# Kernel optimization log

Hardware: AMD Instinct MI355X
Metric: run time of the kernel (lower is better)

The kernel has to match this reference:

```python
import jax, jax.numpy as jnp
import numpy as np

N_NODES = 50000
N_EDGES = 500000
D = 128
R = 8
L = 2
BN_EPS = 1e-5


def setup_inputs() -> dict:
    key = jax.random.key(0)
    ks = jax.random.split(key, 8)
    x = jax.random.normal(ks[0], (N_NODES, D), dtype=jnp.float32)
    xe = jax.random.normal(ks[1], (N_EDGES, D), dtype=jnp.float32)
    edge_index = jax.random.randint(ks[2], (2, N_EDGES), 0, N_NODES, dtype=jnp.int64)
    edge_type = jax.random.randint(ks[3], (N_EDGES,), 0, R, dtype=jnp.int64)
    # glorot init for weight/root, zeros bias; BN affine params
    w_scale = jnp.sqrt(6.0 / (D + D))
    weight = jax.random.uniform(ks[4], (L, R, D, D), jnp.float32, -w_scale, w_scale)
    root = jax.random.uniform(ks[5], (L, D, D), jnp.float32, -w_scale, w_scale)
    bias = jnp.zeros((L, D), jnp.float32)
    bn_gamma = jnp.ones((L, D), jnp.float32)
    bn_beta = jnp.zeros((L, D), jnp.float32)
    return {"x": x, "xe": xe, "edge_index": edge_index, "edge_type": edge_type,
            "weight": weight, "root": root, "bias": bias,
            "bn_gamma": bn_gamma, "bn_beta": bn_beta}


def _rgcn_edge_conv(h, xe, src, dst, etype, w, rt, b):
    # message: relu(x_j + xe) per edge (independent of relation mask)
    m = jax.nn.relu(h[src] + xe)                         # [E, D]
    # mean-aggregate per (relation, dst) via a combined segment id
    n = h.shape[0]
    seg = etype * n + dst                                # [E]
    sums = jax.ops.segment_sum(m, seg, num_segments=R * n)            # [R*N, D]
    cnt = jax.ops.segment_sum(jnp.ones((m.shape[0],), m.dtype), seg,
                              num_segments=R * n)                     # [R*N]
    mean = sums / jnp.maximum(cnt, 1.0)[:, None]
    hr = mean.reshape(R, n, -1)                          # [R, N, D]
    out = jnp.einsum('rnd,rdo->no', hr, w)               # sum_i H_i @ W_i
    out = out + h @ rt + b
    return out


def _batch_norm(h, gamma, beta):
    mu = h.mean(axis=0)
    var = jnp.mean((h - mu) ** 2, axis=0)  # biased, as torch BN (training)
    return (h - mu) * jax.lax.rsqrt(var + BN_EPS) * gamma + beta


def reference(x, xe, edge_index, edge_type, weight, root, bias, bn_gamma, bn_beta):
    src, dst = edge_index[0], edge_index[1]
    h = x
    for l in range(L):
        h = _rgcn_edge_conv(h, xe, src, dst, edge_type, weight[l], root[l], bias[l])
        h = _batch_norm(h, bn_gamma[l], bn_beta[l])
        if l != L - 1:
            h = jax.nn.relu(h)
        # drop_ratio=0 -> dropout is identity
    return h  # JK='last'
```

## Files before the change

### kernel.cpp

```cpp
#include <hip/hip_runtime.h>
#include <hip/hip_bf16.h>

typedef __attribute__((ext_vector_type(8))) short bf16x8;
typedef __attribute__((ext_vector_type(4))) float f32x4;

constexpr int D = 128;
constexpr int R = 8;
constexpr float BN_EPS = 1e-5f;

__device__ __forceinline__ unsigned short f2bf(float x) {
  __hip_bfloat16 b = __float2bfloat16(x);
  union { __hip_bfloat16 b; unsigned short u; } c; c.b = b; return c.u;
}

__global__ __launch_bounds__(256) void hist_k(const int* __restrict__ ei,
                                              const int* __restrict__ et,
                                              int* __restrict__ cnt, int E) {
  int e = blockIdx.x * 256 + threadIdx.x;
  if (e >= E) return;
  atomicAdd(&cnt[ei[E + e] * 8 + et[e]], 1);
}

__global__ __launch_bounds__(256) void scan_partial_k(const int* __restrict__ cnt,
                                                      int* __restrict__ offs,
                                                      int* __restrict__ bsum, int NK) {
  __shared__ int s[256];
  int tid = threadIdx.x;
  int base = blockIdx.x * 4096 + tid * 16;
  int loc[16];
  int sum = 0;
  #pragma unroll
  for (int i = 0; i < 16; ++i) {
    int idx = base + i;
    int v = (idx < NK) ? cnt[idx] : 0;
    loc[i] = sum; sum += v;
  }
  s[tid] = sum;
  __syncthreads();
  if (tid == 0) {
    int run = 0;
    for (int i = 0; i < 256; ++i) { int t = s[i]; s[i] = run; run += t; }
    bsum[blockIdx.x] = run;
  }
  __syncthreads();
  int off = s[tid];
  #pragma unroll
  for (int i = 0; i < 16; ++i) {
    int idx = base + i;
    if (idx < NK) offs[idx] = off + loc[i];
  }
}

__global__ void scan_bsums_k(int* __restrict__ bsum, int nb) {
  if (threadIdx.x == 0 && blockIdx.x == 0) {
    int run = 0;
    for (int b = 0; b < nb; ++b) { int t = bsum[b]; bsum[b] = run; run += t; }
  }
}

__global__ __launch_bounds__(256) void scan_addback_k(int* __restrict__ offs,
                                                      const int* __restrict__ bsum,
                                                      int NK, int E) {
  int idx = blockIdx.x * 256 + threadIdx.x;
  if (idx < NK) offs[idx] += bsum[idx >> 12];
  if (idx == 0) offs[NK] = E;
}

__global__ __launch_bounds__(256) void place_k(const int* __restrict__ ei,
                                               const int* __restrict__ et,
                                               const int* __restrict__ offs,
                                               int* __restrict__ cnt,
                                               int2* __restrict__ pairs, int E) {
  int e = blockIdx.x * 256 + threadIdx.x;
  if (e >= E) return;
  int key = ei[E + e] * 8 + et[e];
  int pos = offs[key] + atomicAdd(&cnt[key], 1);
  pairs[pos] = make_int2(e, ei[e]);
}

__global__ void bnprep_k(const float* __restrict__ colstats,
                         const float* __restrict__ gamma,
                         const float* __restrict__ beta,
                         float* __restrict__ sc, float* __restrict__ sh, int N) {
  int c = threadIdx.x;
  float invN = 1.0f / (float)N;
  float mu = colstats[c] * invN;
  float var = colstats[128 + c] * invN - mu * mu;
  float scale = rsqrtf(var + BN_EPS) * gamma[c];
  sc[c] = scale;
  sh[c] = beta[c] - mu * scale;
}

template <int AFF>
__device__ __forceinline__ void edge_acc(float4& acc, int e, int s, int c,
                                         const float* __restrict__ h,
                                         const float* __restrict__ xe,
                                         const float4 scv, const float4 shv) {
  float4 xv = ((const float4*)xe)[(size_t)e * 32 + c];
  float4 hv = ((const float4*)h)[(size_t)s * 32 + c];
  if (AFF) {
    hv.x = fmaxf(fmaf(hv.x, scv.x, shv.x), 0.f);
    hv.y = fmaxf(fmaf(hv.y, scv.y, shv.y), 0.f);
    hv.z = fmaxf(fmaf(hv.z, scv.z, shv.z), 0.f);
    hv.w = fmaxf(fmaf(hv.w, scv.w, shv.w), 0.f);
  }
  acc.x += fmaxf(xv.x + hv.x, 0.f);
  acc.y += fmaxf(xv.y + hv.y, 0.f);
  acc.z += fmaxf(xv.z + hv.z, 0.f);
  acc.w += fmaxf(xv.w + hv.w, 0.f);
}

template <int AFF>
__global__ __launch_bounds__(256) void agg_k(const float* __restrict__ h,
                                             const float* __restrict__ xe,
                                             const int2* __restrict__ pairs,
                                             const int* __restrict__ offs,
                                             const float* __restrict__ sc,
                                             const float* __restrict__ sh,
                                             unsigned short* __restrict__ Mb,
                                             int NK, int rev) {
  int grp = threadIdx.x >> 5;
  int idx = blockIdx.x * 8 + grp;
  if (idx * 4 >= NK) return;
  if (rev) idx = (NK >> 2) - 1 - idx;
  int s0 = idx * 4;
  int c = threadIdx.x & 31;

  float4 scv = make_float4(0.f, 0.f, 0.f, 0.f), shv = scv;
  if (AFF) {
    scv = *(const float4*)(sc + c * 4);
    shv = *(const float4*)(sh + c * 4);
  }

  int4 ov = *(const int4*)(offs + s0);
  int o4 = offs[s0 + 4];
  int st[4] = {ov.x, ov.y, ov.z, ov.w};
  int en[4] = {ov.y, ov.z, ov.w, o4};

  int2 pr[4];
  #pragma unroll
  for (int j = 0; j < 4; ++j) {
    int m = en[j] - st[j];
    if (m > 0) pr[j] = pairs[st[j] + min(c, min(m, 32) - 1)];
  }

  float4 acc[4];
  #pragma unroll
  for (int j = 0; j < 4; ++j) acc[j] = make_float4(0.f, 0.f, 0.f, 0.f);

#define EP(j, i) edge_acc<AFF>(acc[j], __shfl(pr[j].x, (i), 32), \
                               __shfl(pr[j].y, (i), 32), c, h, xe, scv, shv)

  #pragma unroll
  for (int j = 0; j < 4; ++j) {
    int m = en[j] - st[j];
    if (m > 0) {
      int mm = min(m, 32);
      EP(j, 0);
      if (mm >= 2) EP(j, 1);
      if (mm >= 3) EP(j, 2);
      if (mm >= 4) EP(j, 3);
      for (int i = 4; i < mm; ++i) EP(j, i);
      for (int base = st[j] + 32; base < en[j]; base += 32) {
        int mm2 = min(32, en[j] - base);
        int2 pr2 = pairs[base + min(c, mm2 - 1)];
        for (int i = 0; i < mm2; ++i)
          edge_acc<AFF>(acc[j], __shfl(pr2.x, i, 32), __shfl(pr2.y, i, 32),
                        c, h, xe, scv, shv);
      }
    }
  }
#undef EP

  int pos = (c >> 3) * 32 + (c & 3) * 8 + ((c >> 2) & 1) * 4;
  #pragma unroll
  for (int j = 0; j < 4; ++j) {
    int len = en[j] - st[j];
    float inv = (len > 0) ? 1.0f / (float)len : 0.f;
    ushort4 u;
    u.x = f2bf(acc[j].x * inv); u.y = f2bf(acc[j].y * inv);
    u.z = f2bf(acc[j].z * inv); u.w = f2bf(acc[j].w * inv);
    *(ushort4*)(Mb + (size_t)(s0 + j) * 128 + pos) = u;
  }
}

template <int AFF>
__global__ __launch_bounds__(256) void cast_swz_k(const float* __restrict__ in,
                                                  unsigned short* __restrict__ outb,
                                                  const float* __restrict__ sc,
                                                  const float* __restrict__ sh,
                                                  int n4) {
  int gi = blockIdx.x * 256 + threadIdx.x;
  if (gi >= n4) return;
  int n = gi >> 5, c = gi & 31;
  float4 v = ((const float4*)in)[gi];
  if (AFF) {
    float4 scv = *(const float4*)(sc + c * 4);
    float4 shv = *(const float4*)(sh + c * 4);
    v.x = fmaxf(fmaf(v.x, scv.x, shv.x), 0.f);
    v.y = fmaxf(fmaf(v.y, scv.y, shv.y), 0.f);
    v.z = fmaxf(fmaf(v.z, scv.z, shv.z), 0.f);
    v.w = fmaxf(fmaf(v.w, scv.w, shv.w), 0.f);
  }
  int pos = (c >> 3) * 32 + (c & 3) * 8 + ((c >> 2) & 1) * 4;
  ushort4 u;
  u.x = f2bf(v.x); u.y = f2bf(v.y); u.z = f2bf(v.z); u.w = f2bf(v.w);
  *(ushort4*)(outb + (size_t)n * 128 + pos) = u;
}

__global__ __launch_bounds__(256) void wcast_k(const float* __restrict__ W,
                                               const float* __restrict__ root,
                                               unsigned short* __restrict__ Whi) {
  int idx = blockIdx.x * 256 + threadIdx.x;
  if (idx >= 1152 * 128) return;
  int k = idx >> 7, col = idx & 127;
  float w = (k < 1024) ? W[idx] : root[idx - 1024 * 128];
  int kk = k & 31;
  int pos = (k & ~31) + ((kk & 15) >> 2) * 8 + (kk >> 4) * 4 + (kk & 3);
  Whi[col * 1152 + pos] = f2bf(w);
}

__global__ __launch_bounds__(256) void gemm_k(
    const unsigned short* __restrict__ Mb,
    const unsigned short* __restrict__ hb,
    const unsigned short* __restrict__ Whi,
    const float* __restrict__ bias,
    float* __restrict__ out,
    float* __restrict__ colstats, int N) {
  __shared__ float ldsS[128], ldsQ[128];
  const int tid = threadIdx.x;
  const int wv = tid >> 6, lane = tid & 63;
  const int lr = lane & 15, g = lane >> 4;
  const int r0 = blockIdx.x * 128;
  const int cf0 = wv * 2;

  int row[8];
  #pragma unroll
  for (int rf = 0; rf < 8; ++rf) row[rf] = min(r0 + rf * 16 + lr, N - 1);

  const unsigned short* pb0 = Whi + (size_t)(cf0 * 16 + lr) * 1152 + g * 8;
  const unsigned short* pb1 = pb0 + 16 * 1152;

  f32x4 acc[8][2];
  #pragma unroll
  for (int a = 0; a < 8; ++a)
    #pragma unroll
    for (int b = 0; b < 2; ++b) acc[a][b] = (f32x4){0.f, 0.f, 0.f, 0.f};

  #pragma unroll 2
  for (int t = 0; t < 32; ++t) {
    bf16x8 b0 = *(const bf16x8*)(pb0 + t * 32);
    bf16x8 b1 = *(const bf16x8*)(pb1 + t * 32);
    #pragma unroll
    for (int rf = 0; rf < 8; ++rf) {
      bf16x8 a = *(const bf16x8*)(Mb + (size_t)row[rf] * 1024 + t * 32 + g * 8);
      acc[rf][0] = __builtin_amdgcn_mfma_f32_16x16x32_bf16(a, b0, acc[rf][0], 0, 0, 0);
      acc[rf][1] = __builtin_amdgcn_mfma_f32_16x16x32_bf16(a, b1, acc[rf][1], 0, 0, 0);
    }
  }
  #pragma unroll
  for (int tt = 0; tt < 4; ++tt) {
    bf16x8 b0 = *(const bf16x8*)(pb0 + 1024 + tt * 32);
    bf16x8 b1 = *(const bf16x8*)(pb1 + 1024 + tt * 32);
    #pragma unroll
    for (int rf = 0; rf < 8; ++rf) {
      bf16x8 a = *(const bf16x8*)(hb + (size_t)row[rf] * 128 + tt * 32 + g * 8);
      acc[rf][0] = __builtin_amdgcn_mfma_f32_16x16x32_bf16(a, b0, acc[rf][0], 0, 0, 0);
      acc[rf][1] = __builtin_amdgcn_mfma_f32_16x16x32_bf16(a, b1, acc[rf][1], 0, 0, 0);
    }
  }

  #pragma unroll
  for (int c = 0; c < 2; ++c) {
    int col = (cf0 + c) * 16 + lr;
    float bs = bias[col];
    float s = 0.f, q = 0.f;
    #pragma unroll
    for (int rf = 0; rf < 8; ++rf) {
      #pragma unroll
      for (int j = 0; j < 4; ++j) {
        int r = r0 + rf * 16 + g * 4 + j;
        if (r < N) {
          float v = acc[rf][c][j] + bs;
          out[(size_t)r * 128 + col] = v;
          s += v; q += v * v;
        }
      }
    }
    s += __shfl_xor(s, 16); s += __shfl_xor(s, 32);
    q += __shfl_xor(q, 16); q += __shfl_xor(q, 32);
    if (g == 0) { ldsS[col] = s; ldsQ[col] = q; }
  }
  __syncthreads();
  if (tid < 128) {
    atomicAdd(&colstats[tid], ldsS[tid]);
    atomicAdd(&colstats[128 + tid], ldsQ[tid]);
  }
}

__global__ __launch_bounds__(256) void bn_apply_k(
    const float* __restrict__ in, float* __restrict__ out,
    const float* __restrict__ colstats,
    const float* __restrict__ gamma, const float* __restrict__ beta, int N) {
  int gi = blockIdx.x * 256 + threadIdx.x;
  if (gi >= N * 32) return;
  int c0 = (gi & 31) * 4;
  float invN = 1.0f / (float)N;
  float4 v = ((const float4*)in)[gi];
  float4 o;
  #pragma unroll
  for (int j = 0; j < 4; ++j) {
    int cc = c0 + j;
    float mu = colstats[cc] * invN;
    float var = colstats[128 + cc] * invN - mu * mu;
    float scale = rsqrtf(var + BN_EPS) * gamma[cc];
    float shift = beta[cc] - mu * scale;
    float x = (j == 0) ? v.x : (j == 1) ? v.y : (j == 2) ? v.z : v.w;
    float y = x * scale + shift;
    if (j == 0) o.x = y; else if (j == 1) o.y = y; else if (j == 2) o.z = y; else o.w = y;
  }
  ((float4*)out)[gi] = o;
}

extern "C" void kernel_launch(void* const* d_in, const int* in_sizes, int n_in,
                              void* d_out, int out_size, void* d_ws, size_t ws_size,
                              hipStream_t stream) {
  const float* x      = (const float*)d_in[0];
  const float* xe     = (const float*)d_in[1];
  const int*   ei     = (const int*)d_in[2];
  const int*   et     = (const int*)d_in[3];
  const float* weight = (const float*)d_in[4];
  const float* root   = (const float*)d_in[5];
  const float* bias   = (const float*)d_in[6];
  const float* gamma  = (const float*)d_in[7];
  const float* beta   = (const float*)d_in[8];
  float* out = (float*)d_out;

  const int N = in_sizes[0] / D;
  const int E = in_sizes[3];
  const int NK = N * R;

  char* w = (char*)d_ws;
  size_t off = 0;
  auto alloc = [&](size_t bytes) { char* p = w + off; off = (off + bytes + 255) & ~(size_t)255; return p; };
  unsigned short* Mb   = (unsigned short*)alloc((size_t)NK * 128 * 2);
  unsigned short* hb   = (unsigned short*)alloc((size_t)N * 128 * 2);
  float*          h1   = (float*)alloc((size_t)N * 128 * 4);
  unsigned short* Whi  = (unsigned short*)alloc(1152 * 128 * 2);
  int*            offs = (int*)alloc((size_t)(NK + 1) * 4);
  int*            cnt  = (int*)alloc((size_t)NK * 4);
  int2*           pairs= (int2*)alloc((size_t)E * 8);
  int*            bsum = (int*)alloc(512 * 4);
  float*          cst0 = (float*)alloc(256 * 4);
  float*          cst1 = (float*)alloc(256 * 4);
  float*          sc   = (float*)alloc(128 * 4);
  float*          sh   = (float*)alloc(128 * 4);

  const int NB = (NK + 4095) / 4096;

  hipMemsetAsync(cnt, 0, (size_t)NK * 4, stream);
  hist_k<<<(E + 255) / 256, 256, 0, stream>>>(ei, et, cnt, E);
  scan_partial_k<<<NB, 256, 0, stream>>>(cnt, offs, bsum, NK);
  scan_bsums_k<<<1, 64, 0, stream>>>(bsum, NB);
  scan_addback_k<<<(NK + 255) / 256, 256, 0, stream>>>(offs, bsum, NK, E);
  hipMemsetAsync(cnt, 0, (size_t)NK * 4, stream);
  place_k<<<(E + 255) / 256, 256, 0, stream>>>(ei, et, offs, cnt, pairs, E);

  const int aggBlocks  = (NK + 31) / 32;
  const int gemmBlocks = (N + 127) / 128;
  const int castBlocks = (N * 32 + 255) / 256;

  wcast_k<<<576, 256, 0, stream>>>(weight, root, Whi);
  agg_k<0><<<aggBlocks, 256, 0, stream>>>(x, xe, pairs, offs, nullptr, nullptr,
                                          Mb, NK, 0);
  cast_swz_k<0><<<castBlocks, 256, 0, stream>>>(x, hb, nullptr, nullptr, N * 32);
  hipMemsetAsync(cst0, 0, 256 * 4, stream);
  gemm_k<<<gemmBlocks, 256, 0, stream>>>(Mb, hb, Whi, bias, h1, cst0, N);
  bnprep_k<<<1, 128, 0, stream>>>(cst0, gamma, beta, sc, sh, N);

  wcast_k<<<576, 256, 0, stream>>>(weight + (size_t)1024 * 128,
                                   root + (size_t)128 * 128, Whi);
  agg_k<1><<<aggBlocks, 256, 0, stream>>>(h1, xe, pairs, offs, sc, sh,
                                          Mb, NK, 1 );
  cast_swz_k<1><<<castBlocks, 256, 0, stream>>>(h1, hb, sc, sh, N * 32);
  hipMemsetAsync(cst1, 0, 256 * 4, stream);
  gemm_k<<<gemmBlocks, 256, 0, stream>>>(Mb, hb, Whi, bias + D, out, cst1, N);
  bn_apply_k<<<castBlocks, 256, 0, stream>>>(out, out, cst1, gamma + D, beta + D, N);
}
```

Measured before the change: 477.2 us.

## Gather bf16 swizzled node features in aggregation and process one node per warp-group

The aggregation kernel now gathers source-node features from the bf16, BN-applied, swizzled copy hb, which cast_swz_k already produces. The cast is therefore moved ahead of aggregation, and the per-edge affine and ReLU work disappears. This halves the bytes fetched per random source-row gather. Each 32-lane group now handles all 8 relations of one node instead of 4 segments, which gives more independent loads in flight per group at the cost of extra registers. Messages lose precision because h is rounded to bf16 before the add with xe, which slightly changes numerics.

```diff
diff --git a/kernel.cpp b/kernel.cpp
--- a/kernel.cpp
+++ b/kernel.cpp
@@ -11,6 +11,9 @@
 __device__ __forceinline__ unsigned short f2bf(float x) {
   __hip_bfloat16 b = __float2bfloat16(x);
   union { __hip_bfloat16 b; unsigned short u; } c; c.b = b; return c.u;
+}
+__device__ __forceinline__ float bf2f(unsigned short u) {
+  union { float f; unsigned int i; } c; c.i = ((unsigned int)u) << 16; return c.f;
 }
 
 __global__ __launch_bounds__(256) void hist_k(const int* __restrict__ ei,
@@ -91,68 +94,54 @@
   sh[c] = beta[c] - mu * scale;
 }
 
-template <int AFF>
-__device__ __forceinline__ void edge_acc(float4& acc, int e, int s, int c,
-                                         const float* __restrict__ h,
-                                         const float* __restrict__ xe,
-                                         const float4 scv, const float4 shv) {
+__device__ __forceinline__ void edge_acc(float4& acc, int e, int s, int c, int pos,
+                                         const unsigned short* __restrict__ hb,
+                                         const float* __restrict__ xe) {
   float4 xv = ((const float4*)xe)[(size_t)e * 32 + c];
-  float4 hv = ((const float4*)h)[(size_t)s * 32 + c];
-  if (AFF) {
-    hv.x = fmaxf(fmaf(hv.x, scv.x, shv.x), 0.f);
-    hv.y = fmaxf(fmaf(hv.y, scv.y, shv.y), 0.f);
-    hv.z = fmaxf(fmaf(hv.z, scv.z, shv.z), 0.f);
-    hv.w = fmaxf(fmaf(hv.w, scv.w, shv.w), 0.f);
-  }
-  acc.x += fmaxf(xv.x + hv.x, 0.f);
-  acc.y += fmaxf(xv.y + hv.y, 0.f);
-  acc.z += fmaxf(xv.z + hv.z, 0.f);
-  acc.w += fmaxf(xv.w + hv.w, 0.f);
-}
-
-template <int AFF>
-__global__ __launch_bounds__(256) void agg_k(const float* __restrict__ h,
+  ushort4 hu = *(const ushort4*)(hb + (size_t)s * 128 + pos);
+  acc.x += fmaxf(xv.x + bf2f(hu.x), 0.f);
+  acc.y += fmaxf(xv.y + bf2f(hu.y), 0.f);
+  acc.z += fmaxf(xv.z + bf2f(hu.z), 0.f);
+  acc.w += fmaxf(xv.w + bf2f(hu.w), 0.f);
+}
+
+__global__ __launch_bounds__(256) void agg_k(const unsigned short* __restrict__ hb,
                                              const float* __restrict__ xe,
                                              const int2* __restrict__ pairs,
                                              const int* __restrict__ offs,
-                                             const float* __restrict__ sc,
-                                             const float* __restrict__ sh,
                                              unsigned short* __restrict__ Mb,
                                              int NK, int rev) {
   int grp = threadIdx.x >> 5;
   int idx = blockIdx.x * 8 + grp;
-  if (idx * 4 >= NK) return;
-  if (rev) idx = (NK >> 2) - 1 - idx;
-  int s0 = idx * 4;
+  int nIdx = NK >> 3;
+  if (idx >= nIdx) return;
+  if (rev) idx = nIdx - 1 - idx;
+  int s0 = idx * 8;
   int c = threadIdx.x & 31;
-
-  float4 scv = make_float4(0.f, 0.f, 0.f, 0.f), shv = scv;
-  if (AFF) {
-    scv = *(const float4*)(sc + c * 4);
-    shv = *(const float4*)(sh + c * 4);
-  }
-
-  int4 ov = *(const int4*)(offs + s0);
-  int o4 = offs[s0 + 4];
-  int st[4] = {ov.x, ov.y, ov.z, ov.w};
-  int en[4] = {ov.y, ov.z, ov.w, o4};
-
-  int2 pr[4];
-  #pragma unroll
-  for (int j = 0; j < 4; ++j) {
+  int pos = (c >> 3) * 32 + (c & 3) * 8 + ((c >> 2) & 1) * 4;
+
+  int4 ov0 = *(const int4*)(offs + s0);
+  int4 ov1 = *(const int4*)(offs + s0 + 4);
+  int o8 = offs[s0 + 8];
+  int st[8] = {ov0.x, ov0.y, ov0.z, ov0.w, ov1.x, ov1.y, ov1.z, ov1.w};
+  int en[8] = {ov0.y, ov0.z, ov0.w, ov1.x, ov1.y, ov1.z, ov1.w, o8};
+
+  int2 pr[8];
+  #pragma unroll
+  for (int j = 0; j < 8; ++j) {
     int m = en[j] - st[j];
     if (m > 0) pr[j] = pairs[st[j] + min(c, min(m, 32) - 1)];
   }
 
-  float4 acc[4];
-  #pragma unroll
-  for (int j = 0; j < 4; ++j) acc[j] = make_float4(0.f, 0.f, 0.f, 0.f);
-
-#define EP(j, i) edge_acc<AFF>(acc[j], __shfl(pr[j].x, (i), 32), \
-                               __shfl(pr[j].y, (i), 32), c, h, xe, scv, shv)
-
-  #pragma unroll
-  for (int j = 0; j < 4; ++j) {
+  float4 acc[8];
+  #pragma unroll
+  for (int j = 0; j < 8; ++j) acc[j] = make_float4(0.f, 0.f, 0.f, 0.f);
+
+#define EP(j, i) edge_acc(acc[j], __shfl(pr[j].x, (i), 32), \
+                          __shfl(pr[j].y, (i), 32), c, pos, hb, xe)
+
+  #pragma unroll
+  for (int j = 0; j < 8; ++j) {
     int m = en[j] - st[j];
     if (m > 0) {
       int mm = min(m, 32);
@@ -165,16 +154,15 @@
         int mm2 = min(32, en[j] - base);
         int2 pr2 = pairs[base + min(c, mm2 - 1)];
         for (int i = 0; i < mm2; ++i)
-          edge_acc<AFF>(acc[j], __shfl(pr2.x, i, 32), __shfl(pr2.y, i, 32),
-                        c, h, xe, scv, shv);
+          edge_acc(acc[j], __shfl(pr2.x, i, 32), __shfl(pr2.y, i, 32),
+                   c, pos, hb, xe);
       }
     }
   }
 #undef EP
 
-  int pos = (c >> 3) * 32 + (c & 3) * 8 + ((c >> 2) & 1) * 4;
-  #pragma unroll
-  for (int j = 0; j < 4; ++j) {
+  #pragma unroll
+  for (int j = 0; j < 8; ++j) {
     int len = en[j] - st[j];
     float inv = (len > 0) ? 1.0f / (float)len : 0.f;
     ushort4 u;
@@ -347,7 +335,7 @@
   unsigned short* hb   = (unsigned short*)alloc((size_t)N * 128 * 2);
   float*          h1   = (float*)alloc((size_t)N * 128 * 4);
   unsigned short* Whi  = (unsigned short*)alloc(1152 * 128 * 2);
-  int*            offs = (int*)alloc((size_t)(NK + 1) * 4);
+  int*            offs = (int*)alloc((size_t)(NK + 8) * 4);
   int*            cnt  = (int*)alloc((size_t)NK * 4);
   int2*           pairs= (int2*)alloc((size_t)E * 8);
   int*            bsum = (int*)alloc(512 * 4);
@@ -366,23 +354,21 @@
   hipMemsetAsync(cnt, 0, (size_t)NK * 4, stream);
   place_k<<<(E + 255) / 256, 256, 0, stream>>>(ei, et, offs, cnt, pairs, E);
 
-  const int aggBlocks  = (NK + 31) / 32;
+  const int aggBlocks  = ((NK >> 3) + 7) / 8;
   const int gemmBlocks = (N + 127) / 128;
   const int castBlocks = (N * 32 + 255) / 256;
 
   wcast_k<<<576, 256, 0, stream>>>(weight, root, Whi);
-  agg_k<0><<<aggBlocks, 256, 0, stream>>>(x, xe, pairs, offs, nullptr, nullptr,
-                                          Mb, NK, 0);
   cast_swz_k<0><<<castBlocks, 256, 0, stream>>>(x, hb, nullptr, nullptr, N * 32);
+  agg_k<<<aggBlocks, 256, 0, stream>>>(hb, xe, pairs, offs, Mb, NK, 0);
   hipMemsetAsync(cst0, 0, 256 * 4, stream);
   gemm_k<<<gemmBlocks, 256, 0, stream>>>(Mb, hb, Whi, bias, h1, cst0, N);
   bnprep_k<<<1, 128, 0, stream>>>(cst0, gamma, beta, sc, sh, N);
 
   wcast_k<<<576, 256, 0, stream>>>(weight + (size_t)1024 * 128,
                                    root + (size_t)128 * 128, Whi);
-  agg_k<1><<<aggBlocks, 256, 0, stream>>>(h1, xe, pairs, offs, sc, sh,
-                                          Mb, NK, 1 );
   cast_swz_k<1><<<castBlocks, 256, 0, stream>>>(h1, hb, sc, sh, N * 32);
+  agg_k<<<aggBlocks, 256, 0, stream>>>(hb, xe, pairs, offs, Mb, NK, 1);
   hipMemsetAsync(cst1, 0, 256 * 4, stream);
   gemm_k<<<gemmBlocks, 256, 0, stream>>>(Mb, hb, Whi, bias + D, out, cst1, N);
   bn_apply_k<<<castBlocks, 256, 0, stream>>>(out, out, cst1, gamma + D, beta + D, N);
```

Result: no change. 471.0 us (-1.3%).
